# Optimization experiments

Hardware: AMD Instinct MI355X
Metric: run time of the kernel (lower is better)

The kernel has to match this reference:

```python
import jax, jax.numpy as jnp
import numpy as np

HID = 2048      # hidden_size
H = 16          # num_heads == num_kv_heads (stack in fwd forces MHA)
DH = HID // H   # head_size = 128
QKV = 3 * H * DH  # 6144
THETA = 10000.0
EPS = 1e-5      # flash-attn RMSNorm default eps
B, L = 4, 2048


def setup_inputs() -> dict:
    key = jax.random.key(0)
    k1, k2, k3 = jax.random.split(key, 3)
    hidden_states = jax.random.normal(k1, (B, L, HID), dtype=jnp.float32)
    # weights stored as (in, out); scaled like a typical init so activations stay sane
    W_qkvg = jax.random.normal(k2, (HID, QKV + HID), dtype=jnp.float32) * 0.02
    W_out = jax.random.normal(k3, (HID, HID), dtype=jnp.float32) * 0.02
    return {"hidden_states": hidden_states, "W_qkvg": W_qkvg, "W_out": W_out}


def _rmsnorm(x):
    # elementwise_affine=False: pure rms normalization over head dim
    return x * jax.lax.rsqrt(jnp.mean(x * x, axis=-1, keepdims=True) + EPS)


def _rope(x, seqlen_offset=0):
    # x: (B, L, H, DH), non-interleaved (GPT-NeoX style rotate-half)
    half = DH // 2
    inv_freq = 1.0 / (THETA ** (jnp.arange(half, dtype=jnp.float32) * 2.0 / DH))
    pos = jnp.arange(seqlen_offset, seqlen_offset + x.shape[1], dtype=jnp.float32)
    ang = pos[:, None] * inv_freq[None, :]                  # (L, half)
    cos = jnp.cos(ang)[None, :, None, :]                    # (1,L,1,half)
    sin = jnp.sin(ang)[None, :, None, :]
    x1, x2 = x[..., :half], x[..., half:]
    return jnp.concatenate([x1 * cos - x2 * sin, x1 * sin + x2 * cos], axis=-1)


def _attention_forward(hidden_states, W_qkvg, W_out):
    b, l, _ = hidden_states.shape
    proj = hidden_states @ W_qkvg                           # (B,L,QKV+HID)
    qkv_flat, gate = proj[..., :QKV], proj[..., QKV:]
    gate = jax.nn.sigmoid(gate)
    qkv = qkv_flat.reshape(b, l, 3 * H, DH)
    q, k, v = qkv[:, :, :H], qkv[:, :, H:2 * H], qkv[:, :, 2 * H:]
    q = _rope(_rmsnorm(q))
    k = _rope(_rmsnorm(k))
    # causal softmax attention (math of flash_attn_func)
    scores = jnp.einsum('blhd,bmhd->bhlm', q, k) / np.sqrt(DH).astype(np.float32)
    causal = jnp.tril(jnp.ones((l, l), dtype=bool))
    scores = jnp.where(causal[None, None], scores, jnp.finfo(scores.dtype).min)
    attn = jax.nn.softmax(scores, axis=-1)
    out = jnp.einsum('bhlm,bmhd->blhd', attn, v).reshape(b, l, HID)
    out = out * gate
    return out @ W_out


def reference(hidden_states, W_qkvg, W_out):
    return _attention_forward(hidden_states, W_qkvg, W_out)
```

## Files before the change

kernel.cpp:

```cpp
#include <hip/hip_runtime.h>


typedef __attribute__((ext_vector_type(8))) short bf16x8;
typedef __attribute__((ext_vector_type(4))) float f32x4;
typedef __attribute__((ext_vector_type(4))) unsigned short us4;

#if __has_builtin(__builtin_amdgcn_exp2f)
#define EXP2(x) __builtin_amdgcn_exp2f(x)
#else
#define EXP2(x) exp2f(x)
#endif

__device__ __forceinline__ unsigned short f2bf(float f) {
    unsigned int x = __float_as_uint(f);
    unsigned int r = x + 0x7fffu + ((x >> 16) & 1u);
    return (unsigned short)(r >> 16);
}
__device__ __forceinline__ unsigned short f2bf_fast(float f) {
    return (unsigned short)((__float_as_uint(f) + 0x8000u) >> 16);
}
__device__ __forceinline__ float bf2f(unsigned short u) {
    return __uint_as_float(((unsigned int)u) << 16);
}

__device__ __forceinline__ void gll16(const unsigned short* g, unsigned short* l) {
    __builtin_amdgcn_global_load_lds(
        (const __attribute__((address_space(1))) unsigned int*)g,
        (__attribute__((address_space(3))) unsigned int*)l, 16, 0, 0);
}

__global__ __launch_bounds__(256) void cvt_bf16(const float* __restrict__ in,
                                                unsigned short* __restrict__ out) {
    int i = blockIdx.x * 256 + threadIdx.x;
    float4 v = ((const float4*)in)[i];
    us4 r;
    r[0] = f2bf(v.x); r[1] = f2bf(v.y); r[2] = f2bf(v.z); r[3] = f2bf(v.w);
    ((us4*)out)[i] = r;
}

__global__ __launch_bounds__(256) void transpose_cvt(const float* __restrict__ in,
                                                     unsigned short* __restrict__ out,
                                                     int R, int C) {
    __shared__ float t[32][33];
    int c0 = blockIdx.x * 32, r0 = blockIdx.y * 32;
    int tx = threadIdx.x, ty = threadIdx.y;
#pragma unroll
    for (int i = 0; i < 4; i++)
        t[ty + i * 8][tx] = in[(size_t)(r0 + ty + i * 8) * C + c0 + tx];
    __syncthreads();
#pragma unroll
    for (int i = 0; i < 4; i++)
        out[(size_t)(c0 + ty + i * 8) * R + r0 + tx] = f2bf(t[tx][ty + i * 8]);
}

__global__ __launch_bounds__(256) void transpose_v(const unsigned short* __restrict__ in,
                                                   unsigned short* __restrict__ out) {
    __shared__ unsigned short t[32][33];
    int bh = blockIdx.z, l0 = blockIdx.y * 32, d0 = blockIdx.x * 32;
    int tx = threadIdx.x, ty = threadIdx.y;
    const unsigned short* ib = in + (size_t)bh * 2048 * 128;
    unsigned short* ob = out + (size_t)bh * 128 * 2048;
#pragma unroll
    for (int i = 0; i < 4; i++)
        t[ty + i * 8][tx] = ib[(l0 + ty + i * 8) * 128 + d0 + tx];
    __syncthreads();
#pragma unroll
    for (int i = 0; i < 4; i++)
        ob[(d0 + ty + i * 8) * 2048 + l0 + tx] = t[tx][ty + i * 8];
}

__device__ __forceinline__ void gemm_core(const unsigned short* __restrict__ A,
                                          const unsigned short* __restrict__ Bt,
                                          int K, int rowA0, int colB0,
                                          unsigned short* As, unsigned short* Bs,
                                          f32x4 acc[4][4]) {
    const int tid = threadIdx.x;
    const int w = tid >> 6, lane = tid & 63;
    const int quad = lane >> 4, l15 = lane & 15;
    const int wm = w >> 1, wn = w & 1;
    const int lr = lane >> 3;
    const int lc = ((lane & 7) ^ lr) * 8;

    const unsigned short* ga[4]; const unsigned short* gb[4];
    unsigned short* la[4]; unsigned short* lb[4];
#pragma unroll
    for (int i = 0; i < 4; i++) {
        int r = w * 32 + i * 8;
        ga[i] = A  + (size_t)(rowA0 + r + lr) * K + lc;
        gb[i] = Bt + (size_t)(colB0 + r + lr) * K + lc;
        la[i] = As + r * 64;
        lb[i] = Bs + r * 64;
    }
    const int sw = (l15 & 7);
    const int KT = K >> 6;
    for (int kt = 0; kt < KT; kt++) {
        const int ko = kt * 64;
#pragma unroll
        for (int i = 0; i < 4; i++) gll16(ga[i] + ko, la[i]);
#pragma unroll
        for (int i = 0; i < 4; i++) gll16(gb[i] + ko, lb[i]);
        __syncthreads();
#pragma unroll
        for (int kk = 0; kk < 2; kk++) {
            bf16x8 af[4], bfr[4];
#pragma unroll
            for (int mi = 0; mi < 4; mi++)
                af[mi] = *(const bf16x8*)&As[(wm * 64 + mi * 16 + l15) * 64 +
                                             (((kk * 4 + quad) ^ sw) * 8)];
#pragma unroll
            for (int ni = 0; ni < 4; ni++)
                bfr[ni] = *(const bf16x8*)&Bs[(wn * 64 + ni * 16 + l15) * 64 +
                                              (((kk * 4 + quad) ^ sw) * 8)];
#pragma unroll
            for (int mi = 0; mi < 4; mi++)
#pragma unroll
                for (int ni = 0; ni < 4; ni++)
                    acc[mi][ni] = __builtin_amdgcn_mfma_f32_16x16x32_bf16(
                        af[mi], bfr[ni], acc[mi][ni], 0, 0, 0);
        }
        __syncthreads();
    }
}

__global__ __launch_bounds__(256) void gemm_qkvg(const unsigned short* __restrict__ A,
                                                 const unsigned short* __restrict__ Bt,
                                                 unsigned short* __restrict__ Qb,
                                                 unsigned short* __restrict__ Kb,
                                                 unsigned short* __restrict__ Vb,
                                                 unsigned short* __restrict__ Gb) {
    __shared__ unsigned short As[128 * 64], Bs[128 * 64];
    f32x4 acc[4][4];
    f32x4 z = {0.f, 0.f, 0.f, 0.f};
#pragma unroll
    for (int i = 0; i < 4; i++)
#pragma unroll
        for (int j = 0; j < 4; j++) acc[i][j] = z;

    const int rowA0 = blockIdx.y * 128, colB0 = blockIdx.x * 128;
    gemm_core(A, Bt, 2048, rowA0, colB0, As, Bs, acc);

    const int tid = threadIdx.x, w = tid >> 6, lane = tid & 63;
    const int quad = lane >> 4, l15 = lane & 15;
    const int wm = w >> 1, wn = w & 1;
    const int sec = blockIdx.x >> 4;
    const int h = blockIdx.x & 15;
    unsigned short* dst = (sec == 0) ? Qb : (sec == 1) ? Kb : Vb;
#pragma unroll
    for (int mi = 0; mi < 4; mi++)
#pragma unroll
        for (int ni = 0; ni < 4; ni++)
#pragma unroll
            for (int i = 0; i < 4; i++) {
                int rowg = rowA0 + wm * 64 + mi * 16 + quad * 4 + i;
                int d = wn * 64 + ni * 16 + l15;
                float v = acc[mi][ni][i];
                if (sec < 3) {
                    int b_ = rowg >> 11, l_ = rowg & 2047;
                    dst[(((size_t)(b_ * 16 + h) * 2048 + l_) << 7) + d] = f2bf(v);
                } else {
                    float g = 1.f / (1.f + __expf(-v));
                    Gb[((size_t)rowg << 11) + h * 128 + d] = f2bf(g);
                }
            }
}

__global__ __launch_bounds__(256) void gemm_out(const unsigned short* __restrict__ A,
                                                const unsigned short* __restrict__ Bt,
                                                float* __restrict__ C) {
    __shared__ unsigned short As[128 * 64], Bs[128 * 64];
    f32x4 acc[4][4];
    f32x4 z = {0.f, 0.f, 0.f, 0.f};
#pragma unroll
    for (int i = 0; i < 4; i++)
#pragma unroll
        for (int j = 0; j < 4; j++) acc[i][j] = z;

    const int rowA0 = blockIdx.y * 128, colB0 = blockIdx.x * 128;
    gemm_core(A, Bt, 2048, rowA0, colB0, As, Bs, acc);

    const int tid = threadIdx.x, w = tid >> 6, lane = tid & 63;
    const int quad = lane >> 4, l15 = lane & 15;
    const int wm = w >> 1, wn = w & 1;
#pragma unroll
    for (int mi = 0; mi < 4; mi++)
#pragma unroll
        for (int ni = 0; ni < 4; ni++)
#pragma unroll
            for (int i = 0; i < 4; i++) {
                int rowg = rowA0 + wm * 64 + mi * 16 + quad * 4 + i;
                int col = colB0 + wn * 64 + ni * 16 + l15;
                C[(size_t)rowg * 2048 + col] = acc[mi][ni][i];
            }
}

__global__ __launch_bounds__(256) void rmsnorm_rope(unsigned short* __restrict__ X) {
    const int tid = threadIdx.x;
    const int row = blockIdx.x * 4 + (tid >> 6);
    const int lane = tid & 63;
    unsigned short* p = X + (size_t)row * 128;
    const int l_ = row & 2047;
    float x1 = bf2f(p[lane]);
    float x2 = bf2f(p[lane + 64]);
    float ss = x1 * x1 + x2 * x2;
#pragma unroll
    for (int off = 32; off >= 1; off >>= 1) ss += __shfl_xor(ss, off, 64);
    float r = rsqrtf(ss * (1.f / 128.f) + 1e-5f);
    x1 *= r; x2 *= r;
    float inv = exp2f(-(float)lane * (13.287712379549449f / 64.f));
    float ang = (float)l_ * inv;
    float sn, cs;
    sincosf(ang, &sn, &cs);
    p[lane]      = f2bf(x1 * cs - x2 * sn);
    p[lane + 64] = f2bf(x1 * sn + x2 * cs);
}

__global__ __launch_bounds__(512) void fa_kernel(const unsigned short* __restrict__ Q,
                                                 const unsigned short* __restrict__ K,
                                                 const unsigned short* __restrict__ Vt,
                                                 const unsigned short* __restrict__ G,
                                                 unsigned short* __restrict__ Og) {
    __shared__ unsigned short Ks[64 * 128];
    __shared__ unsigned short Vs[128 * 64];
    __shared__ unsigned short Ps[256 * 64];
    const int g = blockIdx.x;
    const int bh = (g & 7) | ((g >> 6) << 3);
    const int qc = (g >> 3) & 7;
    const int tid = threadIdx.x, w = tid >> 6, lane = tid & 63;
    const int quad = lane >> 4, l15 = lane & 15;
    const int sw = l15 & 7;
    const int qrow0 = qc * 256 + w * 32;
    const float CS = 0.12751740395609812f;

    bf16x8 qf[2][4];
#pragma unroll
    for (int mi = 0; mi < 2; mi++)
#pragma unroll
        for (int kt = 0; kt < 4; kt++)
            qf[mi][kt] = *(const bf16x8*)(Q + ((size_t)bh * 2048 + qrow0 + mi * 16 + l15) * 128
                                             + kt * 32 + quad * 8);

    f32x4 o[2][8];
    f32x4 z = {0.f, 0.f, 0.f, 0.f};
#pragma unroll
    for (int mi = 0; mi < 2; mi++)
#pragma unroll
        for (int nj = 0; nj < 8; nj++) o[mi][nj] = z;
    float rowsum[2][4];
#pragma unroll
    for (int mi = 0; mi < 2; mi++)
#pragma unroll
        for (int i = 0; i < 4; i++) rowsum[mi][i] = 0.f;

    const unsigned short* Kbase = K + (size_t)bh * 2048 * 128;
    const unsigned short* Vtb   = Vt + (size_t)bh * 128 * 2048;

    const int NJ = 4 * (qc + 1);
    for (int j = 0; j < NJ; j++) {
        __syncthreads();

        {
            const int rowoff = lane >> 4, c = lane & 15;
#pragma unroll
            for (int i = 0; i < 2; i++) {
                int r0 = w * 8 + i * 4;
                int row = r0 + rowoff;
                int cs_ = (c & 8) | ((c & 7) ^ (row & 7));
                gll16(Kbase + (size_t)(j * 64 + row) * 128 + cs_ * 8, Ks + r0 * 128);
            }
        }
        {
            const int rowoff = lane >> 3, c = lane & 7;
#pragma unroll
            for (int i = 0; i < 2; i++) {
                int r0 = w * 16 + i * 8;
                int row = r0 + rowoff;
                gll16(Vtb + (size_t)row * 2048 + j * 64 + ((c ^ (row & 7)) * 8),
                      Vs + r0 * 64);
            }
        }
        __syncthreads();

        if (j * 64 >= qrow0 + 32) continue;

        f32x4 s[2][4];
#pragma unroll
        for (int mi = 0; mi < 2; mi++)
#pragma unroll
            for (int nj = 0; nj < 4; nj++) s[mi][nj] = z;
#pragma unroll
        for (int kt = 0; kt < 4; kt++)
#pragma unroll
            for (int nj = 0; nj < 4; nj++) {
                bf16x8 bfr = *(const bf16x8*)&Ks[(nj * 16 + l15) * 128 +
                                                 (((kt * 4 + quad) ^ sw) * 8)];
                s[0][nj] = __builtin_amdgcn_mfma_f32_16x16x32_bf16(qf[0][kt], bfr, s[0][nj], 0, 0, 0);
                s[1][nj] = __builtin_amdgcn_mfma_f32_16x16x32_bf16(qf[1][kt], bfr, s[1][nj], 0, 0, 0);
            }

        const bool diag = (j * 64 + 63 > qrow0);
#pragma unroll
        for (int mi = 0; mi < 2; mi++)
#pragma unroll
            for (int nj = 0; nj < 4; nj++)
#pragma unroll
                for (int i = 0; i < 4; i++) {
                    float pp = EXP2(s[mi][nj][i] * CS);
                    int row_l = mi * 16 + quad * 4 + i;
                    if (diag) {
                        int col_g = j * 64 + nj * 16 + l15;
                        if (col_g > qrow0 + row_l) pp = 0.f;
                    }
                    rowsum[mi][i] += pp;
                    int kv = nj * 16 + l15;
                    Ps[(w * 32 + row_l) * 64 + (((kv >> 3) ^ (row_l & 7)) * 8) + (kv & 7)] =
                        f2bf_fast(pp);
                }

#pragma unroll
        for (int ktl = 0; ktl < 2; ktl++) {
            bf16x8 a0 = *(const bf16x8*)&Ps[(w * 32 + l15) * 64 +
                                            (((ktl * 4 + quad) ^ sw) * 8)];
            bf16x8 a1 = *(const bf16x8*)&Ps[(w * 32 + 16 + l15) * 64 +
                                            (((ktl * 4 + quad) ^ sw) * 8)];
#pragma unroll
            for (int nj = 0; nj < 8; nj++) {
                bf16x8 bfr = *(const bf16x8*)&Vs[(nj * 16 + l15) * 64 +
                                                 (((ktl * 4 + quad) ^ sw) * 8)];
                o[0][nj] = __builtin_amdgcn_mfma_f32_16x16x32_bf16(a0, bfr, o[0][nj], 0, 0, 0);
                o[1][nj] = __builtin_amdgcn_mfma_f32_16x16x32_bf16(a1, bfr, o[1][nj], 0, 0, 0);
            }
        }
    }

    const int b_ = bh >> 4, h = bh & 15;
#pragma unroll
    for (int mi = 0; mi < 2; mi++)
#pragma unroll
        for (int i = 0; i < 4; i++) {
            float t = rowsum[mi][i];
#pragma unroll
            for (int off = 1; off < 16; off <<= 1) t += __shfl_xor(t, off, 16);
            float rl = 1.f / t;
            int l_ = qrow0 + mi * 16 + quad * 4 + i;
#pragma unroll
            for (int nj = 0; nj < 8; nj++) {
                int d = nj * 16 + l15;
                size_t gi = ((size_t)(b_ * 2048 + l_) * 2048) + h * 128 + d;
                Og[gi] = f2bf(o[mi][nj][i] * rl * bf2f(G[gi]));
            }
        }
}

extern "C" void kernel_launch(void* const* d_in, const int* in_sizes, int n_in,
                              void* d_out, int out_size, void* d_ws, size_t ws_size,
                              hipStream_t stream) {
    const float* X  = (const float*)d_in[0];
    const float* Wq = (const float*)d_in[1];
    const float* Wo = (const float*)d_in[2];
    float* out = (float*)d_out;

    char* ws = (char*)d_ws;
    const size_t SZ = 33554432ull;
    unsigned short* Xb  = (unsigned short*)(ws);
    unsigned short* Wqt = (unsigned short*)(ws + SZ);
    unsigned short* Wot = (unsigned short*)(ws + 2 * SZ);
    unsigned short* Qb  = (unsigned short*)(ws + 2 * SZ + 8388608ull);
    unsigned short* Kb  = (unsigned short*)(ws + 3 * SZ + 8388608ull);
    unsigned short* Vb  = (unsigned short*)(ws + 4 * SZ + 8388608ull);
    unsigned short* Gb  = (unsigned short*)(ws + 5 * SZ + 8388608ull);
    unsigned short* Vt  = Wqt;
    unsigned short* OG  = Xb;

    cvt_bf16<<<16384, 256, 0, stream>>>(X, Xb);
    transpose_cvt<<<dim3(256, 64), dim3(32, 8), 0, stream>>>(Wq, Wqt, 2048, 8192);
    transpose_cvt<<<dim3(64, 64),  dim3(32, 8), 0, stream>>>(Wo, Wot, 2048, 2048);

    gemm_qkvg<<<dim3(64, 64), 256, 0, stream>>>(Xb, Wqt, Qb, Kb, Vb, Gb);

    rmsnorm_rope<<<32768, 256, 0, stream>>>(Qb);
    rmsnorm_rope<<<32768, 256, 0, stream>>>(Kb);
    transpose_v<<<dim3(4, 64, 64), dim3(32, 8), 0, stream>>>(Vb, Vt);

    fa_kernel<<<512, 512, 0, stream>>>(Qb, Kb, Vt, Gb, OG);

    gemm_out<<<dim3(16, 64), 256, 0, stream>>>(OG, Wot, out);
}
```

Before: 807.8 us.

## Fuse V transpose into QKV GEMM epilogue and shrink attention P buffer

The QKV projection GEMM now writes V already transposed, staging it through a swizzled shared-memory tile and storing 16-byte vectors. This removes the separate transpose_v kernel and its extra global round trip. The two RMSNorm+RoPE launches are merged into one 2D-grid launch. In the attention kernel, P is written and consumed in two 32-column halves so the P shared buffer is halved, and a minimum-blocks launch bound of 6 is added to aim for higher occupancy, with some risk of register spilling.

```diff
diff --git a/kernel.cpp b/kernel.cpp
--- a/kernel.cpp
+++ b/kernel.cpp
@@ -51,22 +51,6 @@
 #pragma unroll
     for (int i = 0; i < 4; i++)
         out[(size_t)(c0 + ty + i * 8) * R + r0 + tx] = f2bf(t[tx][ty + i * 8]);
-}
-
-__global__ __launch_bounds__(256) void transpose_v(const unsigned short* __restrict__ in,
-                                                   unsigned short* __restrict__ out) {
-    __shared__ unsigned short t[32][33];
-    int bh = blockIdx.z, l0 = blockIdx.y * 32, d0 = blockIdx.x * 32;
-    int tx = threadIdx.x, ty = threadIdx.y;
-    const unsigned short* ib = in + (size_t)bh * 2048 * 128;
-    unsigned short* ob = out + (size_t)bh * 128 * 2048;
-#pragma unroll
-    for (int i = 0; i < 4; i++)
-        t[ty + i * 8][tx] = ib[(l0 + ty + i * 8) * 128 + d0 + tx];
-    __syncthreads();
-#pragma unroll
-    for (int i = 0; i < 4; i++)
-        ob[(d0 + ty + i * 8) * 2048 + l0 + tx] = t[tx][ty + i * 8];
 }
 
 __device__ __forceinline__ void gemm_core(const unsigned short* __restrict__ A,
@@ -126,9 +110,11 @@
                                                  const unsigned short* __restrict__ Bt,
                                                  unsigned short* __restrict__ Qb,
                                                  unsigned short* __restrict__ Kb,
-                                                 unsigned short* __restrict__ Vb,
+                                                 unsigned short* __restrict__ Vt,
                                                  unsigned short* __restrict__ Gb) {
-    __shared__ unsigned short As[128 * 64], Bs[128 * 64];
+    __shared__ unsigned short smem[128 * 128];
+    unsigned short* As = smem;
+    unsigned short* Bs = smem + 128 * 64;
     f32x4 acc[4][4];
     f32x4 z = {0.f, 0.f, 0.f, 0.f};
 #pragma unroll
@@ -144,24 +130,57 @@
     const int wm = w >> 1, wn = w & 1;
     const int sec = blockIdx.x >> 4;
     const int h = blockIdx.x & 15;
-    unsigned short* dst = (sec == 0) ? Qb : (sec == 1) ? Kb : Vb;
-#pragma unroll
-    for (int mi = 0; mi < 4; mi++)
-#pragma unroll
-        for (int ni = 0; ni < 4; ni++)
-#pragma unroll
-            for (int i = 0; i < 4; i++) {
-                int rowg = rowA0 + wm * 64 + mi * 16 + quad * 4 + i;
-                int d = wn * 64 + ni * 16 + l15;
-                float v = acc[mi][ni][i];
-                if (sec < 3) {
-                    int b_ = rowg >> 11, l_ = rowg & 2047;
-                    dst[(((size_t)(b_ * 16 + h) * 2048 + l_) << 7) + d] = f2bf(v);
-                } else {
-                    float g = 1.f / (1.f + __expf(-v));
+
+    if (sec == 2) {
+#pragma unroll
+        for (int mi = 0; mi < 4; mi++)
+#pragma unroll
+            for (int ni = 0; ni < 4; ni++)
+#pragma unroll
+                for (int i = 0; i < 4; i++) {
+                    int ll = wm * 64 + mi * 16 + quad * 4 + i;
+                    int d  = wn * 64 + ni * 16 + l15;
+                    smem[d * 128 + (((ll >> 3) ^ (d & 15)) * 8) + (ll & 7)] =
+                        f2bf(acc[mi][ni][i]);
+                }
+        __syncthreads();
+        const int b_ = rowA0 >> 11, l0 = rowA0 & 2047;
+        const int r = tid >> 1, hf = tid & 1;
+        unsigned short* drow = Vt + (size_t)(b_ * 16 + h) * 128 * 2048 +
+                               (size_t)r * 2048 + l0;
+#pragma unroll
+        for (int jj = 0; jj < 8; jj++) {
+            int jcol = hf * 8 + jj;
+            *(bf16x8*)(drow + jcol * 8) =
+                *(const bf16x8*)&smem[r * 128 + ((jcol ^ (r & 15)) * 8)];
+        }
+    } else if (sec == 3) {
+#pragma unroll
+        for (int mi = 0; mi < 4; mi++)
+#pragma unroll
+            for (int ni = 0; ni < 4; ni++)
+#pragma unroll
+                for (int i = 0; i < 4; i++) {
+                    int rowg = rowA0 + wm * 64 + mi * 16 + quad * 4 + i;
+                    int d = wn * 64 + ni * 16 + l15;
+                    float g = 1.f / (1.f + __expf(-acc[mi][ni][i]));
                     Gb[((size_t)rowg << 11) + h * 128 + d] = f2bf(g);
                 }
-            }
+    } else {
+        unsigned short* dst = (sec == 0) ? Qb : Kb;
+#pragma unroll
+        for (int mi = 0; mi < 4; mi++)
+#pragma unroll
+            for (int ni = 0; ni < 4; ni++)
+#pragma unroll
+                for (int i = 0; i < 4; i++) {
+                    int rowg = rowA0 + wm * 64 + mi * 16 + quad * 4 + i;
+                    int d = wn * 64 + ni * 16 + l15;
+                    int b_ = rowg >> 11, l_ = rowg & 2047;
+                    dst[(((size_t)(b_ * 16 + h) * 2048 + l_) << 7) + d] =
+                        f2bf(acc[mi][ni][i]);
+                }
+    }
 }
 
 __global__ __launch_bounds__(256) void gemm_out(const unsigned short* __restrict__ A,
@@ -193,7 +212,9 @@
             }
 }
 
-__global__ __launch_bounds__(256) void rmsnorm_rope(unsigned short* __restrict__ X) {
+__global__ __launch_bounds__(256) void rmsnorm_rope(unsigned short* __restrict__ Qp,
+                                                    unsigned short* __restrict__ Kp) {
+    unsigned short* X = blockIdx.y ? Kp : Qp;
     const int tid = threadIdx.x;
     const int row = blockIdx.x * 4 + (tid >> 6);
     const int lane = tid & 63;
@@ -214,14 +235,14 @@
     p[lane + 64] = f2bf(x1 * sn + x2 * cs);
 }
 
-__global__ __launch_bounds__(512) void fa_kernel(const unsigned short* __restrict__ Q,
-                                                 const unsigned short* __restrict__ K,
-                                                 const unsigned short* __restrict__ Vt,
-                                                 const unsigned short* __restrict__ G,
-                                                 unsigned short* __restrict__ Og) {
+__global__ __launch_bounds__(512, 6) void fa_kernel(const unsigned short* __restrict__ Q,
+                                                    const unsigned short* __restrict__ K,
+                                                    const unsigned short* __restrict__ Vt,
+                                                    const unsigned short* __restrict__ G,
+                                                    unsigned short* __restrict__ Og) {
     __shared__ unsigned short Ks[64 * 128];
     __shared__ unsigned short Vs[128 * 64];
-    __shared__ unsigned short Ps[256 * 64];
+    __shared__ unsigned short Ps[256 * 32];
     const int g = blockIdx.x;
     const int bh = (g & 7) | ((g >> 6) << 3);
     const int qc = (g >> 3) & 7;
@@ -254,6 +275,9 @@
     const unsigned short* Kbase = K + (size_t)bh * 2048 * 128;
     const unsigned short* Vtb   = Vt + (size_t)bh * 128 * 2048;
 
+    const int pr0 = w * 32 + l15, pr1 = pr0 + 16;
+    const int pk0 = (pr0 >> 1) & 3, pk1 = (pr1 >> 1) & 3;
+
     const int NJ = 4 * (qc + 1);
     for (int j = 0; j < NJ; j++) {
         __syncthreads();
@@ -299,33 +323,33 @@
 
         const bool diag = (j * 64 + 63 > qrow0);
 #pragma unroll
-        for (int mi = 0; mi < 2; mi++)
-#pragma unroll
-            for (int nj = 0; nj < 4; nj++)
-#pragma unroll
-                for (int i = 0; i < 4; i++) {
-                    float pp = EXP2(s[mi][nj][i] * CS);
-                    int row_l = mi * 16 + quad * 4 + i;
-                    if (diag) {
-                        int col_g = j * 64 + nj * 16 + l15;
-                        if (col_g > qrow0 + row_l) pp = 0.f;
+        for (int hh = 0; hh < 2; hh++) {
+#pragma unroll
+            for (int mi = 0; mi < 2; mi++)
+#pragma unroll
+                for (int njh = 0; njh < 2; njh++) {
+                    const int nj = hh * 2 + njh;
+#pragma unroll
+                    for (int i = 0; i < 4; i++) {
+                        float pp = EXP2(s[mi][nj][i] * CS);
+                        int row_l = mi * 16 + quad * 4 + i;
+                        if (diag) {
+                            int col_g = j * 64 + nj * 16 + l15;
+                            if (col_g > qrow0 + row_l) pp = 0.f;
+                        }
+                        rowsum[mi][i] += pp;
+                        int row = w * 32 + row_l;
+                        int kv = njh * 16 + l15;
+                        Ps[row * 32 + ((((kv >> 3) ^ ((row >> 1) & 3)) * 8)) + (kv & 7)] =
+                            f2bf_fast(pp);
                     }
-                    rowsum[mi][i] += pp;
-                    int kv = nj * 16 + l15;
-                    Ps[(w * 32 + row_l) * 64 + (((kv >> 3) ^ (row_l & 7)) * 8) + (kv & 7)] =
-                        f2bf_fast(pp);
                 }
-
-#pragma unroll
-        for (int ktl = 0; ktl < 2; ktl++) {
-            bf16x8 a0 = *(const bf16x8*)&Ps[(w * 32 + l15) * 64 +
-                                            (((ktl * 4 + quad) ^ sw) * 8)];
-            bf16x8 a1 = *(const bf16x8*)&Ps[(w * 32 + 16 + l15) * 64 +
-                                            (((ktl * 4 + quad) ^ sw) * 8)];
+            bf16x8 a0 = *(const bf16x8*)&Ps[pr0 * 32 + ((quad ^ pk0) * 8)];
+            bf16x8 a1 = *(const bf16x8*)&Ps[pr1 * 32 + ((quad ^ pk1) * 8)];
 #pragma unroll
             for (int nj = 0; nj < 8; nj++) {
                 bf16x8 bfr = *(const bf16x8*)&Vs[(nj * 16 + l15) * 64 +
-                                                 (((ktl * 4 + quad) ^ sw) * 8)];
+                                                 (((hh * 4 + quad) ^ sw) * 8)];
                 o[0][nj] = __builtin_amdgcn_mfma_f32_16x16x32_bf16(a0, bfr, o[0][nj], 0, 0, 0);
                 o[1][nj] = __builtin_amdgcn_mfma_f32_16x16x32_bf16(a1, bfr, o[1][nj], 0, 0, 0);
             }
@@ -366,20 +390,17 @@
     unsigned short* Wot = (unsigned short*)(ws + 2 * SZ);
     unsigned short* Qb  = (unsigned short*)(ws + 2 * SZ + 8388608ull);
     unsigned short* Kb  = (unsigned short*)(ws + 3 * SZ + 8388608ull);
-    unsigned short* Vb  = (unsigned short*)(ws + 4 * SZ + 8388608ull);
+    unsigned short* Vt  = (unsigned short*)(ws + 4 * SZ + 8388608ull);
     unsigned short* Gb  = (unsigned short*)(ws + 5 * SZ + 8388608ull);
-    unsigned short* Vt  = Wqt;
     unsigned short* OG  = Xb;
 
     cvt_bf16<<<16384, 256, 0, stream>>>(X, Xb);
     transpose_cvt<<<dim3(256, 64), dim3(32, 8), 0, stream>>>(Wq, Wqt, 2048, 8192);
     transpose_cvt<<<dim3(64, 64),  dim3(32, 8), 0, stream>>>(Wo, Wot, 2048, 2048);
 
-    gemm_qkvg<<<dim3(64, 64), 256, 0, stream>>>(Xb, Wqt, Qb, Kb, Vb, Gb);
-
-    rmsnorm_rope<<<32768, 256, 0, stream>>>(Qb);
-    rmsnorm_rope<<<32768, 256, 0, stream>>>(Kb);
-    transpose_v<<<dim3(4, 64, 64), dim3(32, 8), 0, stream>>>(Vb, Vt);
+    gemm_qkvg<<<dim3(64, 64), 256, 0, stream>>>(Xb, Wqt, Qb, Kb, Vt, Gb);
+
+    rmsnorm_rope<<<dim3(32768, 2), 256, 0, stream>>>(Qb, Kb);
 
     fa_kernel<<<512, 512, 0, stream>>>(Qb, Kb, Vt, Gb, OG);
 
```

Result: slower. 1.809 ms (+123.9%).
